# Kernel tuning notes

Measured on AMD Instinct MI355X. Metric: run time of the kernel, lower is better.

Reference implementation:

```python
import jax, jax.numpy as jnp
import numpy as np

SAMPLE_RATE = 24000
THRESHOLD_FACTOR = 5.0
MAX_SPIKE_SAMPLES = int(0.0015 * SAMPLE_RATE)  # 36
K_MAX = 65536  # static upper bound on number of threshold crossings
N_SAMPLES = 24_000_000


def setup_inputs() -> dict:
    key = jax.random.key(0)
    x = jax.random.normal(key, (N_SAMPLES,), dtype=jnp.float32)
    return {"data_detected": x}


def _detect_one(v, threshold):
    """Detect peaks of v above +threshold. For the negative pass, call with -x
    (x < -thr  <=>  -x > thr, and argmin(x) == argmax(-x)). Returns an int32
    array of length K_MAX: valid peak indices first (sorted), padded with -1."""
    N = v.shape[0]
    mask = (v > threshold).astype(jnp.int32)
    d = jnp.diff(mask)  # +1 = entry (False->True), -1 = exit (True->False)
    entries = jnp.nonzero(d == 1, size=K_MAX, fill_value=N)[0]
    exits = jnp.nonzero(d == -1, size=K_MAX, fill_value=N)[0]
    n = jnp.minimum(jnp.sum(d == 1), jnp.sum(d == -1))
    idx = jnp.arange(K_MAX)
    dur = exits - entries
    keep = (idx < n) & (dur <= MAX_SPIKE_SAMPLES)
    # vectorized windowed peak search: (K_MAX, W) gather + row argmax
    win_idx = jnp.clip(entries[:, None] + jnp.arange(MAX_SPIKE_SAMPLES)[None, :], 0, N - 1)
    windows = v[win_idx]
    peaks = entries + jnp.argmax(windows, axis=1)
    # compact valid peaks to the front (entries are sorted), pad with -1
    peaks = jnp.sort(jnp.where(keep, peaks, N))
    total = jnp.sum(keep)
    return jnp.where(idx < total, peaks, -1)


def reference(data_detected):
    x = data_detected
    threshold = THRESHOLD_FACTOR * jnp.median(jnp.abs(x)) / 0.6745
    pos_indices = _detect_one(x, threshold)
    neg_indices = _detect_one(-x, threshold)
    return pos_indices, neg_indices, threshold
```

## Files before the change

### kernel.cpp

```cpp
#include <hip/hip_runtime.h>
#include <stdint.h>

#define HB 18
#define SH_SIZE 8192
#define NSAMP 65536
#define SMARG 1912
#define DBITS 22
#define CAND_CAP 8192
#define CSORT_CAP 4096
#define CBUF_CAP 256
#define LIST_CAP 2500000
#define LBUF_CAP 4096
#define PAIR_CAP 512
#define PEAK_CAP 512
#define MAX_SPIKE 36
#define AB_BLOCKS 128

#define P_ULO   0
#define P_UHI   1
#define P_THRLO 2
#define P_THR   3
#define P_CANDN 4
#define P_LISTN 5
#define P_CB    6
#define P_BINA1 7
#define P_BINA2 8
#define P_RA1   9
#define P_RA2   10
#define P_DONES 11
#define P_DONEA 12
#define P_DONEB 13

#define WS_SHIST  0
#define WS_HISTA  32768
#define WS_HISTB  40960
#define WS_PARAMS 57344
#define WS_ZERO_BYTES 57408
#define WS_CAND   57600
#define WS_LIST   102400

__global__ __launch_bounds__(256) void k_prep(int* __restrict__ ws, int nInts,
                                              float* __restrict__ out, int n2) {
  int j = blockIdx.x * 256 + threadIdx.x;
  if (j < nInts) ws[j] = 0;
  if (j < n2) out[j] = -1.0f;
}

__global__ __launch_bounds__(256) void k_sample(const float* __restrict__ x, int N,
                                                int* __restrict__ shist,
                                                int* __restrict__ p) {
  __shared__ int h[SH_SIZE];
  __shared__ int lastS;
  __shared__ int part[256];
  __shared__ int excl[256];
  __shared__ uint32_t uLoS, uHiS;
  int tid = threadIdx.x;
  for (int i = tid; i < SH_SIZE; i += 256) h[i] = 0;
  __syncthreads();
  int stride = N / NSAMP; if (stride < 1) stride = 1;
  for (int i = blockIdx.x * 256 + tid; i < NSAMP; i += gridDim.x * 256) {
    long long idx = (long long)i * stride;
    if (idx < N) {
      uint32_t u = __float_as_uint(x[idx]) & 0x7fffffffu;
      atomicAdd(&h[u >> HB], 1);
    }
  }
  __syncthreads();
  for (int i = tid; i < SH_SIZE; i += 256) {
    int c = h[i];
    if (c) atomicAdd(&shist[i], c);
  }
  __threadfence();
  if (tid == 0) lastS = (atomicAdd(&p[P_DONES], 1) == (int)gridDim.x - 1);
  __syncthreads();
  if (!lastS) return;
  __threadfence();
  const int chunk = SH_SIZE / 256;
  int base = tid * chunk;
  int s = 0;
  int cc[chunk];
  for (int w = 0; w < chunk; ++w) { cc[w] = shist[base + w]; s += cc[w]; }
  part[tid] = s;
  __syncthreads();
  if (tid == 0) { int a = 0; for (int i = 0; i < 256; ++i) { excl[i] = a; a += part[i]; } }
  __syncthreads();
  int pre = excl[tid];
  int sA = NSAMP / 2 - SMARG, sB = NSAMP / 2 + SMARG;
  if (pre <= sA && sA < pre + s) {
    int a = pre;
    for (int w = 0; w < chunk; ++w) {
      if (sA < a + cc[w]) { uLoS = (uint32_t)(base + w) << HB; break; }
      a += cc[w];
    }
  }
  if (pre <= sB && sB < pre + s) {
    int a = pre;
    for (int w = 0; w < chunk; ++w) {
      if (sB < a + cc[w]) { uHiS = (uint32_t)(base + w + 1) << HB; break; }
      a += cc[w];
    }
  }
  __syncthreads();
  if (tid == 0) {
    uint32_t uLo = uLoS, uHi = uHiS;
    if (uHi - uLo > (1u << DBITS)) uHi = uLo + (1u << DBITS);
    p[P_ULO] = (int)uLo;
    p[P_UHI] = (int)uHi;
    float vLo = __uint_as_float(uLo);
    p[P_THRLO] = __float_as_int((5.0f * vLo / 0.6745f) * 0.999f);
  }
}

__device__ inline void m_elem(uint32_t fbits, int idx, uint32_t uLo, uint32_t bw,
                              uint32_t thrBits, int* lbuf, int* lcnt,
                              int* cbuf, int* ccnt, int& cb) {
  uint32_t u = fbits & 0x7fffffffu;
  cb += (u < uLo) ? 1 : 0;
  if (u - uLo < bw) {
    int id = atomicAdd(lcnt, 1);
    if (id < LBUF_CAP) lbuf[id] = (int)(u - uLo);
  }
  if (u > thrBits) {
    int id = atomicAdd(ccnt, 1);
    if (id < CBUF_CAP) cbuf[id] = idx;
  }
}

__global__ __launch_bounds__(256) void k_main(const float* __restrict__ x, int N,
                                              int* __restrict__ p,
                                              int* __restrict__ list,
                                              int* __restrict__ cand) {
  __shared__ int lbuf[LBUF_CAP];
  __shared__ int cbuf[CBUF_CAP];
  __shared__ int red[256];
  __shared__ int lcnt, ccnt, lbase, cbase;
  int tid = threadIdx.x;
  if (tid == 0) { lcnt = 0; ccnt = 0; }
  __syncthreads();
  uint32_t uLo = (uint32_t)p[P_ULO];
  uint32_t bw  = (uint32_t)p[P_UHI] - uLo;
  uint32_t thrBits = (uint32_t)p[P_THRLO];
  int cb = 0;
  int NV = N >> 2;
  int str = gridDim.x * 256;
  const uint4* vec = reinterpret_cast<const uint4*>(x);
  int j = blockIdx.x * 256 + tid;
  for (; j + 7 * str < NV; j += 8 * str) {
    uint4 v[8];
#pragma unroll
    for (int k = 0; k < 8; ++k) v[k] = vec[j + k * str];
#pragma unroll
    for (int k = 0; k < 8; ++k) {
      int base = (j + k * str) << 2;
      m_elem(v[k].x, base + 0, uLo, bw, thrBits, lbuf, &lcnt, cbuf, &ccnt, cb);
      m_elem(v[k].y, base + 1, uLo, bw, thrBits, lbuf, &lcnt, cbuf, &ccnt, cb);
      m_elem(v[k].z, base + 2, uLo, bw, thrBits, lbuf, &lcnt, cbuf, &ccnt, cb);
      m_elem(v[k].w, base + 3, uLo, bw, thrBits, lbuf, &lcnt, cbuf, &ccnt, cb);
    }
  }
  for (; j < NV; j += str) {
    uint4 a = vec[j];
    int base = j << 2;
    m_elem(a.x, base + 0, uLo, bw, thrBits, lbuf, &lcnt, cbuf, &ccnt, cb);
    m_elem(a.y, base + 1, uLo, bw, thrBits, lbuf, &lcnt, cbuf, &ccnt, cb);
    m_elem(a.z, base + 2, uLo, bw, thrBits, lbuf, &lcnt, cbuf, &ccnt, cb);
    m_elem(a.w, base + 3, uLo, bw, thrBits, lbuf, &lcnt, cbuf, &ccnt, cb);
  }
  if (blockIdx.x == 0 && tid == 0) {
    for (int i = NV << 2; i < N; ++i)
      m_elem(__float_as_uint(x[i]), i, uLo, bw, thrBits, lbuf, &lcnt, cbuf, &ccnt, cb);
  }
  __syncthreads();
  int nl = lcnt < LBUF_CAP ? lcnt : LBUF_CAP;
  int nc = ccnt < CBUF_CAP ? ccnt : CBUF_CAP;
  if (tid == 0) {
    lbase = atomicAdd(&p[P_LISTN], nl);
    cbase = atomicAdd(&p[P_CANDN], nc);
  }
  red[tid] = cb;
  __syncthreads();
  for (int s2 = 128; s2; s2 >>= 1) {
    if (tid < s2) red[tid] += red[tid + s2];
    __syncthreads();
  }
  if (tid == 0) atomicAdd(&p[P_CB], red[0]);
  for (int i = tid; i < nl; i += 256)
    if (lbase + i < LIST_CAP) list[lbase + i] = lbuf[i];
  for (int i = tid; i < nc; i += 256)
    if (cbase + i < CAND_CAP) cand[cbase + i] = cbuf[i];
}

__global__ __launch_bounds__(256) void k_stageA(const int* __restrict__ list,
                                                int* __restrict__ p,
                                                int* __restrict__ histA, int N) {
  __shared__ int h[2048];
  __shared__ int lastS;
  __shared__ int part[256];
  __shared__ int excl[256];
  int tid = threadIdx.x;
  for (int i = tid; i < 2048; i += 256) h[i] = 0;
  __syncthreads();
  int n = p[P_LISTN]; if (n > LIST_CAP) n = LIST_CAP;
  int str = gridDim.x * 256;
  for (int i = blockIdx.x * 256 + tid; i < n; i += str)
    atomicAdd(&h[list[i] >> 11], 1);
  __syncthreads();
  for (int i = tid; i < 2048; i += 256) {
    int c = h[i];
    if (c) atomicAdd(&histA[i], c);
  }
  __threadfence();
  if (tid == 0) lastS = (atomicAdd(&p[P_DONEA], 1) == (int)gridDim.x - 1);
  __syncthreads();
  if (!lastS) return;
  __threadfence();
  long long k1 = (long long)(N / 2) - 1, k2 = (long long)(N / 2);
  long long cb = p[P_CB];
  long long r1l = k1 - cb, r2l = k2 - cb;
  if (r1l < 0) r1l = 0; if (r1l > n - 1) r1l = n - 1;
  if (r2l < 0) r2l = 0; if (r2l > n - 1) r2l = n - 1;
  int r1 = (int)r1l, r2 = (int)r2l;
  int base = tid * 8;
  int cc[8]; int s = 0;
#pragma unroll
  for (int w = 0; w < 8; ++w) { cc[w] = histA[base + w]; s += cc[w]; }
  part[tid] = s;
  __syncthreads();
  if (tid == 0) { int a = 0; for (int i = 0; i < 256; ++i) { excl[i] = a; a += part[i]; } }
  __syncthreads();
  int pre = excl[tid];
  if (pre <= r1 && r1 < pre + s) {
    int a = pre;
    for (int w = 0; w < 8; ++w) {
      if (r1 < a + cc[w]) { p[P_BINA1] = base + w; p[P_RA1] = r1 - a; break; }
      a += cc[w];
    }
  }
  if (pre <= r2 && r2 < pre + s) {
    int a = pre;
    for (int w = 0; w < 8; ++w) {
      if (r2 < a + cc[w]) { p[P_BINA2] = base + w; p[P_RA2] = r2 - a; break; }
      a += cc[w];
    }
  }
}

__device__ static void isort(int* a, int n) {
  for (int i = 1; i < n; ++i) {
    int v = a[i]; int j = i - 1;
    while (j >= 0 && a[j] > v) { a[j + 1] = a[j]; --j; }
    a[j + 1] = v;
  }
}

__device__ inline void eval_pair(const float* __restrict__ x, int p, float thr,
                                 int* pe, int* px, int* ne, int* nx, int* cnt) {
  float a = x[p], b = x[p + 1];
  bool m0 = a > thr, m1 = b > thr;
  if (m0 != m1) {
    int id = atomicAdd(&cnt[m1 ? 0 : 1], 1);
    if (id < PAIR_CAP) (m1 ? pe : px)[id] = p;
  }
  bool q0 = (-a) > thr, q1 = (-b) > thr;
  if (q0 != q1) {
    int id = atomicAdd(&cnt[q1 ? 2 : 3], 1);
    if (id < PAIR_CAP) (q1 ? ne : nx)[id] = p;
  }
}

__device__ inline int wave_argmax36(const float* __restrict__ x, int N, int sign,
                                    int e, int lane) {
  float val = -INFINITY;
  int wi = lane;
  if (lane < MAX_SPIKE) {
    int idx = e + lane; if (idx > N - 1) idx = N - 1;
    float v = x[idx];
    val = (sign < 0) ? -v : v;
  }
  for (int off = 32; off; off >>= 1) {
    float ov = __shfl_xor(val, off);
    int owi = __shfl_xor(wi, off);
    if (ov > val || (ov == val && owi < wi)) { val = ov; wi = owi; }
  }
  return e + wi;
}

__device__ inline int proc_pol(const float* __restrict__ x, int N, int sign,
                               const int* eL, int nE, const int* xL, int nX,
                               int* pk, int lane) {
  int n = nE < nX ? nE : nX;
  int tot = 0;
  for (int t = 0; t < n; ++t) {
    int dur = xL[t] - eL[t];
    if (dur <= MAX_SPIKE) {
      int pp = wave_argmax36(x, N, sign, eL[t], lane);
      if (tot < PEAK_CAP && lane == 0) pk[tot] = pp;
      ++tot;
    }
  }
  if (tot > PEAK_CAP) tot = PEAK_CAP;
  if (lane == 0) isort(pk, tot);
  return tot;
}

__global__ __launch_bounds__(256) void k_stageB(const float* __restrict__ x, int N,
                                                const int* __restrict__ list,
                                                int* __restrict__ p,
                                                int* __restrict__ histB,
                                                int* __restrict__ cand,
                                                float* __restrict__ out, int OUT_K) {
  __shared__ int h[4096];
  __shared__ int lastS;
  __shared__ int part[256];
  __shared__ int excl[256];
  __shared__ float vres[2];
  __shared__ float sthr;
  __shared__ int cl[CSORT_CAP];
  __shared__ int pe[PAIR_CAP], px[PAIR_CAP], ne[PAIR_CAP], nx[PAIR_CAP];
  __shared__ int cnt[4];
  __shared__ int pkP[PEAK_CAP], pkN[PEAK_CAP];
  __shared__ int nPk[2];
  int tid = threadIdx.x;
  for (int i = tid; i < 4096; i += 256) h[i] = 0;
  __syncthreads();
  int n = p[P_LISTN]; if (n > LIST_CAP) n = LIST_CAP;
  int binA1 = p[P_BINA1], binA2 = p[P_BINA2];
  int str = gridDim.x * 256;
  for (int i = blockIdx.x * 256 + tid; i < n; i += str) {
    int d = list[i];
    int hi = d >> 11, lo = d & 2047;
    if (hi == binA1) atomicAdd(&h[lo], 1);
    if (hi == binA2) atomicAdd(&h[2048 + lo], 1);
  }
  __syncthreads();
  for (int i = tid; i < 4096; i += 256) {
    int c = h[i];
    if (c) atomicAdd(&histB[i], c);
  }
  __threadfence();
  if (tid == 0) lastS = (atomicAdd(&p[P_DONEB], 1) == (int)gridDim.x - 1);
  __syncthreads();
  if (!lastS) return;
  __threadfence();
  uint32_t uLo = (uint32_t)p[P_ULO];
  if (tid < 2) vres[tid] = __uint_as_float(uLo);
  for (int tgt = 0; tgt < 2; ++tgt) {
    __syncthreads();
    const int* hh = histB + tgt * 2048;
    int rank = (tgt == 0) ? p[P_RA1] : p[P_RA2];
    int binA = (tgt == 0) ? binA1 : binA2;
    int base = tid * 8;
    int cc[8]; int s = 0;
#pragma unroll
    for (int w = 0; w < 8; ++w) { cc[w] = hh[base + w]; s += cc[w]; }
    part[tid] = s;
    __syncthreads();
    if (tid == 0) { int a = 0; for (int i = 0; i < 256; ++i) { excl[i] = a; a += part[i]; } }
    __syncthreads();
    int pre = excl[tid];
    if (pre <= rank && rank < pre + s) {
      int a = pre;
      for (int w = 0; w < 8; ++w) {
        if (rank < a + cc[w]) {
          uint32_t bits = uLo + ((uint32_t)binA << 11) + (uint32_t)(base + w);
          vres[tgt] = __uint_as_float(bits);
          break;
        }
        a += cc[w];
      }
    }
  }
  __syncthreads();
  if (tid == 0) {
    float med = 0.5f * (vres[0] + vres[1]);
    float thr = (5.0f * med) / 0.6745f;
    p[P_THR] = __float_as_int(thr);
    sthr = thr;
    out[2 * OUT_K] = thr;
  }
  if (tid < 4) cnt[tid] = 0;
  __syncthreads();
  float thr = sthr;
  int nC = p[P_CANDN]; if (nC > CAND_CAP) nC = CAND_CAP;
  const int* cnd;
  if (nC <= CSORT_CAP) {
    for (int i = tid; i < nC; i += 256) cl[i] = cand[i];
    __syncthreads();
    int myv[CSORT_CAP / 256], myr[CSORT_CAP / 256], nh = 0;
    for (int i = tid; i < nC; i += 256) {
      int v = cl[i];
      int r = 0;
      for (int q = 0; q < nC; ++q) r += (cl[q] < v) ? 1 : 0;
      myv[nh] = v; myr[nh] = r; ++nh;
    }
    __syncthreads();
    for (int t = 0; t < nh; ++t) cl[myr[t]] = myv[t];
    __syncthreads();
    cnd = cl;
  } else {
    if (tid == 0) isort(cand, nC);
    __syncthreads();
    cnd = cand;
  }
  for (int k = tid; k < nC; k += 256) {
    int c = cnd[k];
    bool prevAdj = (k > 0) && (cnd[k - 1] == c - 1);
    if (c > 0 && !prevAdj) eval_pair(x, c - 1, thr, pe, px, ne, nx, cnt);
    if (c <= N - 2) eval_pair(x, c, thr, pe, px, ne, nx, cnt);
  }
  __syncthreads();
  int nPE = min(cnt[0], PAIR_CAP), nPX = min(cnt[1], PAIR_CAP);
  int nNE = min(cnt[2], PAIR_CAP), nNX = min(cnt[3], PAIR_CAP);
  if (tid == 0) { isort(pe, nPE); isort(px, nPX); }
  else if (tid == 1) { isort(ne, nNE); isort(nx, nNX); }
  __syncthreads();
  if (tid < 64) {
    int t0 = proc_pol(x, N, +1, pe, nPE, px, nPX, pkP, tid);
    int t1 = proc_pol(x, N, -1, ne, nNE, nx, nNX, pkN, tid);
    if (tid == 0) { nPk[0] = t0; nPk[1] = t1; }
  }
  __syncthreads();
  for (int j = tid; j < nPk[0]; j += 256) out[j] = (float)pkP[j];
  for (int j = tid; j < nPk[1]; j += 256) out[OUT_K + j] = (float)pkN[j];
}

extern "C" void kernel_launch(void* const* d_in, const int* in_sizes, int n_in,
                              void* d_out, int out_size, void* d_ws, size_t ws_size,
                              hipStream_t stream) {
  const float* x = (const float*)d_in[0];
  int N = in_sizes[0];
  float* out = (float*)d_out;
  char* ws = (char*)d_ws;

  int* shist  = (int*)(ws + WS_SHIST);
  int* histA  = (int*)(ws + WS_HISTA);
  int* histB  = (int*)(ws + WS_HISTB);
  int* params = (int*)(ws + WS_PARAMS);
  int* cand   = (int*)(ws + WS_CAND);
  int* list   = (int*)(ws + WS_LIST);

  int OUT_K = (out_size - 1) / 2;
  int nInts = WS_ZERO_BYTES / 4;
  int prepN = 2 * OUT_K;

  k_prep<<<(prepN + 255) / 256, 256, 0, stream>>>((int*)ws, nInts, out, prepN);
  k_sample<<<64, 256, 0, stream>>>(x, N, shist, params);
  k_main<<<2048, 256, 0, stream>>>(x, N, params, list, cand);
  k_stageA<<<AB_BLOCKS, 256, 0, stream>>>(list, params, histA, N);
  k_stageB<<<AB_BLOCKS, 256, 0, stream>>>(x, N, list, params, histB, cand, out, OUT_K);
}
```

Before: 173.2 us.

## Fuse stage-A histogram into main pass and use wave-aggregated LDS atomics

Builds the stage-A coarse histogram of the median band inside the main streaming kernel, so the separate k_stageA launch and its re-read of the list buffer go away. The last block still picks the two median bins. Per-element shared-memory atomics are replaced with ballot-based wave-aggregated pushes. The main pass is split into two launches over the two halves of the input, one with the old strided pattern and one with contiguous 2048-vector tiles. The sampling kernel now reads the first 65536 contiguous samples instead of a strided subsample, which trades representativeness for cheaper access. It also shrinks the LDS list buffer, which raises the risk of overflow.

```diff
diff --git a/kernel.cpp b/kernel.cpp
--- a/kernel.cpp
+++ b/kernel.cpp
@@ -10,11 +10,12 @@
 #define CSORT_CAP 4096
 #define CBUF_CAP 256
 #define LIST_CAP 2500000
-#define LBUF_CAP 4096
+#define LBUF_CAP 3072
 #define PAIR_CAP 512
 #define PEAK_CAP 512
 #define MAX_SPIKE 36
 #define AB_BLOCKS 128
+#define MAIN_G 1024
 
 #define P_ULO   0
 #define P_UHI   1
@@ -57,11 +58,9 @@
   int tid = threadIdx.x;
   for (int i = tid; i < SH_SIZE; i += 256) h[i] = 0;
   __syncthreads();
-  int stride = N / NSAMP; if (stride < 1) stride = 1;
   for (int i = blockIdx.x * 256 + tid; i < NSAMP; i += gridDim.x * 256) {
-    long long idx = (long long)i * stride;
-    if (idx < N) {
-      uint32_t u = __float_as_uint(x[idx]) & 0x7fffffffu;
+    if (i < N) {
+      uint32_t u = __float_as_uint(x[i]) & 0x7fffffffu;
       atomicAdd(&h[u >> HB], 1);
     }
   }
@@ -111,112 +110,71 @@
   }
 }
 
-__device__ inline void m_elem(uint32_t fbits, int idx, uint32_t uLo, uint32_t bw,
-                              uint32_t thrBits, int* lbuf, int* lcnt,
-                              int* cbuf, int* ccnt, int& cb) {
+__device__ __forceinline__ void push_agg(bool pred, int val, int lane,
+                                         int* buf, int* cnt, int cap) {
+  unsigned long long bm = __ballot(pred);
+  if (bm) {
+    int total = __popcll(bm);
+    int prefix = __popcll(bm & ((1ull << lane) - 1ull));
+    int leader = __builtin_ctzll(bm);
+    int base = 0;
+    if (lane == leader) base = atomicAdd(cnt, total);
+    base = __shfl(base, leader);
+    if (pred) {
+      int id = base + prefix;
+      if (id < cap) buf[id] = val;
+    }
+  }
+}
+
+__device__ __forceinline__ void m_elem(uint32_t fbits, int idx, uint32_t uLo, uint32_t bw,
+                                       uint32_t thrBits, int lane,
+                                       int* lbuf, int* lcnt, int* cbuf, int* ccnt, int& cb) {
   uint32_t u = fbits & 0x7fffffffu;
   cb += (u < uLo) ? 1 : 0;
-  if (u - uLo < bw) {
-    int id = atomicAdd(lcnt, 1);
-    if (id < LBUF_CAP) lbuf[id] = (int)(u - uLo);
-  }
-  if (u > thrBits) {
-    int id = atomicAdd(ccnt, 1);
-    if (id < CBUF_CAP) cbuf[id] = idx;
-  }
-}
-
-__global__ __launch_bounds__(256) void k_main(const float* __restrict__ x, int N,
-                                              int* __restrict__ p,
-                                              int* __restrict__ list,
-                                              int* __restrict__ cand) {
-  __shared__ int lbuf[LBUF_CAP];
-  __shared__ int cbuf[CBUF_CAP];
-  __shared__ int red[256];
-  __shared__ int lcnt, ccnt, lbase, cbase;
-  int tid = threadIdx.x;
-  if (tid == 0) { lcnt = 0; ccnt = 0; }
-  __syncthreads();
-  uint32_t uLo = (uint32_t)p[P_ULO];
-  uint32_t bw  = (uint32_t)p[P_UHI] - uLo;
-  uint32_t thrBits = (uint32_t)p[P_THRLO];
-  int cb = 0;
-  int NV = N >> 2;
-  int str = gridDim.x * 256;
-  const uint4* vec = reinterpret_cast<const uint4*>(x);
-  int j = blockIdx.x * 256 + tid;
-  for (; j + 7 * str < NV; j += 8 * str) {
-    uint4 v[8];
-#pragma unroll
-    for (int k = 0; k < 8; ++k) v[k] = vec[j + k * str];
-#pragma unroll
-    for (int k = 0; k < 8; ++k) {
-      int base = (j + k * str) << 2;
-      m_elem(v[k].x, base + 0, uLo, bw, thrBits, lbuf, &lcnt, cbuf, &ccnt, cb);
-      m_elem(v[k].y, base + 1, uLo, bw, thrBits, lbuf, &lcnt, cbuf, &ccnt, cb);
-      m_elem(v[k].z, base + 2, uLo, bw, thrBits, lbuf, &lcnt, cbuf, &ccnt, cb);
-      m_elem(v[k].w, base + 3, uLo, bw, thrBits, lbuf, &lcnt, cbuf, &ccnt, cb);
-    }
-  }
-  for (; j < NV; j += str) {
-    uint4 a = vec[j];
-    int base = j << 2;
-    m_elem(a.x, base + 0, uLo, bw, thrBits, lbuf, &lcnt, cbuf, &ccnt, cb);
-    m_elem(a.y, base + 1, uLo, bw, thrBits, lbuf, &lcnt, cbuf, &ccnt, cb);
-    m_elem(a.z, base + 2, uLo, bw, thrBits, lbuf, &lcnt, cbuf, &ccnt, cb);
-    m_elem(a.w, base + 3, uLo, bw, thrBits, lbuf, &lcnt, cbuf, &ccnt, cb);
-  }
-  if (blockIdx.x == 0 && tid == 0) {
-    for (int i = NV << 2; i < N; ++i)
-      m_elem(__float_as_uint(x[i]), i, uLo, bw, thrBits, lbuf, &lcnt, cbuf, &ccnt, cb);
-  }
-  __syncthreads();
-  int nl = lcnt < LBUF_CAP ? lcnt : LBUF_CAP;
-  int nc = ccnt < CBUF_CAP ? ccnt : CBUF_CAP;
+  push_agg(u - uLo < bw, (int)(u - uLo), lane, lbuf, lcnt, LBUF_CAP);
+  push_agg(u > thrBits, idx, lane, cbuf, ccnt, CBUF_CAP);
+}
+
+__device__ void block_tail(int tid, int G2, int cb, int N,
+                           int* lbuf, int* cbuf, int* red, int* histA_l,
+                           int* part, int* excl,
+                           int* lcntP, int* ccntP,
+                           int* p, int* list, int* cand, int* histA) {
+  __shared__ int lbase, cbase, lastS;
+  __syncthreads();
+  int nl = *lcntP; if (nl > LBUF_CAP) nl = LBUF_CAP;
+  int nc = *ccntP; if (nc > CBUF_CAP) nc = CBUF_CAP;
+  for (int i = tid; i < nl; i += 256) atomicAdd(&histA_l[lbuf[i] >> 11], 1);
+  red[tid] = cb;
+  __syncthreads();
+  for (int s2 = 128; s2; s2 >>= 1) {
+    if (tid < s2) red[tid] += red[tid + s2];
+    __syncthreads();
+  }
   if (tid == 0) {
     lbase = atomicAdd(&p[P_LISTN], nl);
     cbase = atomicAdd(&p[P_CANDN], nc);
-  }
-  red[tid] = cb;
-  __syncthreads();
-  for (int s2 = 128; s2; s2 >>= 1) {
-    if (tid < s2) red[tid] += red[tid + s2];
-    __syncthreads();
-  }
-  if (tid == 0) atomicAdd(&p[P_CB], red[0]);
+    atomicAdd(&p[P_CB], red[0]);
+  }
+  __syncthreads();
   for (int i = tid; i < nl; i += 256)
     if (lbase + i < LIST_CAP) list[lbase + i] = lbuf[i];
   for (int i = tid; i < nc; i += 256)
     if (cbase + i < CAND_CAP) cand[cbase + i] = cbuf[i];
-}
-
-__global__ __launch_bounds__(256) void k_stageA(const int* __restrict__ list,
-                                                int* __restrict__ p,
-                                                int* __restrict__ histA, int N) {
-  __shared__ int h[2048];
-  __shared__ int lastS;
-  __shared__ int part[256];
-  __shared__ int excl[256];
-  int tid = threadIdx.x;
-  for (int i = tid; i < 2048; i += 256) h[i] = 0;
-  __syncthreads();
-  int n = p[P_LISTN]; if (n > LIST_CAP) n = LIST_CAP;
-  int str = gridDim.x * 256;
-  for (int i = blockIdx.x * 256 + tid; i < n; i += str)
-    atomicAdd(&h[list[i] >> 11], 1);
-  __syncthreads();
   for (int i = tid; i < 2048; i += 256) {
-    int c = h[i];
+    int c = histA_l[i];
     if (c) atomicAdd(&histA[i], c);
   }
   __threadfence();
-  if (tid == 0) lastS = (atomicAdd(&p[P_DONEA], 1) == (int)gridDim.x - 1);
+  if (tid == 0) lastS = (atomicAdd(&p[P_DONEA], 1) == G2 - 1);
   __syncthreads();
   if (!lastS) return;
   __threadfence();
+  int n = p[P_LISTN]; if (n > LIST_CAP) n = LIST_CAP;
   long long k1 = (long long)(N / 2) - 1, k2 = (long long)(N / 2);
-  long long cb = p[P_CB];
-  long long r1l = k1 - cb, r2l = k2 - cb;
+  long long cbAll = p[P_CB];
+  long long r1l = k1 - cbAll, r2l = k2 - cbAll;
   if (r1l < 0) r1l = 0; if (r1l > n - 1) r1l = n - 1;
   if (r2l < 0) r2l = 0; if (r2l > n - 1) r2l = n - 1;
   int r1 = (int)r1l, r2 = (int)r2l;
@@ -243,6 +201,108 @@
       a += cc[w];
     }
   }
+}
+
+__global__ __launch_bounds__(256) void k_mainS(const float* __restrict__ x, int N,
+                                               int vLo, int vHi, int G2,
+                                               int* __restrict__ p,
+                                               int* __restrict__ list,
+                                               int* __restrict__ cand,
+                                               int* __restrict__ histA) {
+  __shared__ int lbuf[LBUF_CAP];
+  __shared__ int cbuf[CBUF_CAP];
+  __shared__ int red[256];
+  __shared__ int histA_l[2048];
+  __shared__ int part[256];
+  __shared__ int excl[256];
+  __shared__ int lcnt, ccnt;
+  int tid = threadIdx.x, lane = tid & 63;
+  if (tid == 0) { lcnt = 0; ccnt = 0; }
+  for (int i = tid; i < 2048; i += 256) histA_l[i] = 0;
+  __syncthreads();
+  uint32_t uLo = (uint32_t)p[P_ULO];
+  uint32_t bw  = (uint32_t)p[P_UHI] - uLo;
+  uint32_t thrBits = (uint32_t)p[P_THRLO];
+  int cb = 0;
+  int str = gridDim.x * 256;
+  const uint4* vec = reinterpret_cast<const uint4*>(x);
+  int j = vLo + blockIdx.x * 256 + tid;
+  for (; j + 7 * str < vHi; j += 8 * str) {
+    uint4 v[8];
+#pragma unroll
+    for (int k = 0; k < 8; ++k) v[k] = vec[j + k * str];
+#pragma unroll
+    for (int k = 0; k < 8; ++k) {
+      int eb = (j + k * str) << 2;
+      m_elem(v[k].x, eb + 0, uLo, bw, thrBits, lane, lbuf, &lcnt, cbuf, &ccnt, cb);
+      m_elem(v[k].y, eb + 1, uLo, bw, thrBits, lane, lbuf, &lcnt, cbuf, &ccnt, cb);
+      m_elem(v[k].z, eb + 2, uLo, bw, thrBits, lane, lbuf, &lcnt, cbuf, &ccnt, cb);
+      m_elem(v[k].w, eb + 3, uLo, bw, thrBits, lane, lbuf, &lcnt, cbuf, &ccnt, cb);
+    }
+  }
+  for (; j < vHi; j += str) {
+    uint4 a = vec[j];
+    int ei = j << 2;
+    m_elem(a.x, ei + 0, uLo, bw, thrBits, lane, lbuf, &lcnt, cbuf, &ccnt, cb);
+    m_elem(a.y, ei + 1, uLo, bw, thrBits, lane, lbuf, &lcnt, cbuf, &ccnt, cb);
+    m_elem(a.z, ei + 2, uLo, bw, thrBits, lane, lbuf, &lcnt, cbuf, &ccnt, cb);
+    m_elem(a.w, ei + 3, uLo, bw, thrBits, lane, lbuf, &lcnt, cbuf, &ccnt, cb);
+  }
+  block_tail(tid, G2, cb, N, lbuf, cbuf, red, histA_l, part, excl,
+             &lcnt, &ccnt, p, list, cand, histA);
+}
+
+__global__ __launch_bounds__(256) void k_mainC(const float* __restrict__ x, int N,
+                                               int vLo, int vHi, int G2,
+                                               int* __restrict__ p,
+                                               int* __restrict__ list,
+                                               int* __restrict__ cand,
+                                               int* __restrict__ histA) {
+  __shared__ int lbuf[LBUF_CAP];
+  __shared__ int cbuf[CBUF_CAP];
+  __shared__ int red[256];
+  __shared__ int histA_l[2048];
+  __shared__ int part[256];
+  __shared__ int excl[256];
+  __shared__ int lcnt, ccnt;
+  int tid = threadIdx.x, lane = tid & 63;
+  if (tid == 0) { lcnt = 0; ccnt = 0; }
+  for (int i = tid; i < 2048; i += 256) histA_l[i] = 0;
+  __syncthreads();
+  uint32_t uLo = (uint32_t)p[P_ULO];
+  uint32_t bw  = (uint32_t)p[P_UHI] - uLo;
+  uint32_t thrBits = (uint32_t)p[P_THRLO];
+  int cb = 0;
+  const uint4* vec = reinterpret_cast<const uint4*>(x);
+  int nT = (vHi - vLo) >> 11;
+  for (int t = blockIdx.x; t < nT; t += gridDim.x) {
+    int basev = vLo + (t << 11) + tid;
+    uint4 v[8];
+#pragma unroll
+    for (int k = 0; k < 8; ++k) v[k] = vec[basev + (k << 8)];
+#pragma unroll
+    for (int k = 0; k < 8; ++k) {
+      int eb = (basev + (k << 8)) << 2;
+      m_elem(v[k].x, eb + 0, uLo, bw, thrBits, lane, lbuf, &lcnt, cbuf, &ccnt, cb);
+      m_elem(v[k].y, eb + 1, uLo, bw, thrBits, lane, lbuf, &lcnt, cbuf, &ccnt, cb);
+      m_elem(v[k].z, eb + 2, uLo, bw, thrBits, lane, lbuf, &lcnt, cbuf, &ccnt, cb);
+      m_elem(v[k].w, eb + 3, uLo, bw, thrBits, lane, lbuf, &lcnt, cbuf, &ccnt, cb);
+    }
+  }
+  for (int j = vLo + (nT << 11) + blockIdx.x * 256 + tid; j < vHi; j += gridDim.x * 256) {
+    uint4 a = vec[j];
+    int ei = j << 2;
+    m_elem(a.x, ei + 0, uLo, bw, thrBits, lane, lbuf, &lcnt, cbuf, &ccnt, cb);
+    m_elem(a.y, ei + 1, uLo, bw, thrBits, lane, lbuf, &lcnt, cbuf, &ccnt, cb);
+    m_elem(a.z, ei + 2, uLo, bw, thrBits, lane, lbuf, &lcnt, cbuf, &ccnt, cb);
+    m_elem(a.w, ei + 3, uLo, bw, thrBits, lane, lbuf, &lcnt, cbuf, &ccnt, cb);
+  }
+  if (blockIdx.x == 0 && tid == 0) {
+    for (int i2 = vHi << 2; i2 < N; ++i2)
+      m_elem(__float_as_uint(x[i2]), i2, uLo, bw, thrBits, lane, lbuf, &lcnt, cbuf, &ccnt, cb);
+  }
+  block_tail(tid, G2, cb, N, lbuf, cbuf, red, histA_l, part, excl,
+             &lcnt, &ccnt, p, list, cand, histA);
 }
 
 __device__ static void isort(int* a, int n) {
@@ -443,9 +503,13 @@
   int nInts = WS_ZERO_BYTES / 4;
   int prepN = 2 * OUT_K;
 
+  int NV = N >> 2;
+  int NVh = (NV / 2) & ~2047;
+  int G2 = 2 * MAIN_G;
+
   k_prep<<<(prepN + 255) / 256, 256, 0, stream>>>((int*)ws, nInts, out, prepN);
   k_sample<<<64, 256, 0, stream>>>(x, N, shist, params);
-  k_main<<<2048, 256, 0, stream>>>(x, N, params, list, cand);
-  k_stageA<<<AB_BLOCKS, 256, 0, stream>>>(list, params, histA, N);
+  k_mainS<<<MAIN_G, 256, 0, stream>>>(x, N, 0, NVh, G2, params, list, cand, histA);
+  k_mainC<<<MAIN_G, 256, 0, stream>>>(x, N, NVh, NV, G2, params, list, cand, histA);
   k_stageB<<<AB_BLOCKS, 256, 0, stream>>>(x, N, list, params, histB, cand, out, OUT_K);
 }
```

After: 294.9 us. 70.2% more time.
